# Performance work log

Measured on AMD Instinct MI355X. Metric: run time of the kernel, lower is better.

## Reference

```python
import jax, jax.numpy as jnp
import numpy as np
import math

KERNEL_SIZE = 11
SIGMA = 1.0
STABILIZATION = 1e-06


def _gauss_kernel(k, sigma):
    pad = k // 2
    coords = jnp.arange(k, dtype=jnp.float32) - pad
    yy, xx = jnp.meshgrid(coords, coords, indexing='ij')
    g = jnp.exp(-(xx ** 2 + yy ** 2) / (2.0 * sigma ** 2))
    return g / g.sum()


def _depthwise_gauss(x, g):
    # x: [B, C, H, W]; g: [K, K]. Zero 'SAME' padding matches nn.Unfold(padding=K//2).
    C = x.shape[1]
    k = g.shape[0]
    w = jnp.broadcast_to(g[None, None], (C, 1, k, k)).astype(x.dtype)
    return jax.lax.conv_general_dilated(
        x, w, window_strides=(1, 1), padding='SAME',
        feature_group_count=C,
        dimension_numbers=('NCHW', 'OIHW', 'NCHW'))


def setup_inputs() -> dict:
    key = jax.random.key(0)
    x = jax.random.normal(key, (16, 64, 256, 256), dtype=jnp.float32)
    return {"x": x}


def reference(x):
    g = _gauss_kernel(KERNEL_SIZE, SIGMA)
    # Weighted local mean and second moment; since sum(g)=1:
    # var = E_w[x^2] - (E_w[x])^2  ==  sum_w (x - mean)^2  (same math as the torch module)
    mean = _depthwise_gauss(x, g)
    ex2 = _depthwise_gauss(x * x, g)
    var = ex2 - mean * mean + STABILIZATION
    return jnp.sqrt(var)
```

## Files before the change

kernel.cpp:

```cpp
#include <hip/hip_runtime.h>
#include <math.h>


#define W        256
#define IMG_PIX  (W * W)
#define BANDH    64
#define LDSW     272

#define GW0 1.4867195e-06f
#define GW1 1.3383023e-04f
#define GW2 4.4318485e-03f
#define GW3 5.3990965e-02f
#define GW4 2.4197072e-01f
#define GW5 3.9894228e-01f

__device__ __forceinline__ float4 f4add(float4 a, float4 b) {
    return make_float4(a.x + b.x, a.y + b.y, a.z + b.z, a.w + b.w);
}
__device__ __forceinline__ float4 f4mul(float4 a, float4 b) {
    return make_float4(a.x * b.x, a.y * b.y, a.z * b.z, a.w * b.w);
}
__device__ __forceinline__ float4 f4scale(float g, float4 a) {
    return make_float4(g * a.x, g * a.y, g * a.z, g * a.w);
}
__device__ __forceinline__ float4 f4fma(float g, float4 a, float4 b) {
    return make_float4(fmaf(g, a.x, b.x), fmaf(g, a.y, b.y),
                       fmaf(g, a.z, b.z), fmaf(g, a.w, b.w));
}

__device__ __forceinline__ void lds_fence_hard() {
    __asm__ volatile("s_waitcnt lgkmcnt(0)" ::: "memory");
}
__device__ __forceinline__ void lds_fence_order() {
    __asm__ volatile("" ::: "memory");
}

__device__ __forceinline__ float4 load_row(const float* __restrict__ xi, int gr, int c) {
    if ((unsigned)gr < (unsigned)W)
        return *(const float4*)(xi + (size_t)gr * W + c);
    return make_float4(0.f, 0.f, 0.f, 0.f);
}

__device__ __forceinline__ void hconv4(float4 q0, float4 q1, float4 q2,
                                       float4 q3, float4 q4, float h[4]) {
    float f[20] = { q0.x, q0.y, q0.z, q0.w,  q1.x, q1.y, q1.z, q1.w,
                    q2.x, q2.y, q2.z, q2.w,  q3.x, q3.y, q3.z, q3.w,
                    q4.x, q4.y, q4.z, q4.w };
    #pragma unroll
    for (int j = 0; j < 4; ++j) {
        float s = GW5 * f[j + 8];
        s = fmaf(GW4, f[j + 7] + f[j + 9],  s);
        s = fmaf(GW3, f[j + 6] + f[j + 10], s);
        s = fmaf(GW2, f[j + 5] + f[j + 11], s);
        s = fmaf(GW1, f[j + 4] + f[j + 12], s);
        s = fmaf(GW0, f[j + 3] + f[j + 13], s);
        h[j] = s;
    }
}

template<int K>
__device__ __forceinline__ void row_step(const float* __restrict__ xi,
                                         float* __restrict__ oi,
                                         float4 (&xw)[11], float4& pf,
                                         float* __restrict__ b1,
                                         float* __restrict__ b2,
                                         int c, int grow) {
    constexpr int SN = (K + 10) % 11;
    xw[SN] = pf;
    float4 pn = load_row(xi, grow + 6, c);

    constexpr int SC = (K + 5) % 11;
    float4 xc = xw[SC];
    float4 v1 = f4scale(GW5, xc);
    float4 v2 = f4scale(GW5, f4mul(xc, xc));
    #define VPAIR(D, G) { constexpr int A_ = (K + 5 - (D)) % 11;                    \
                          constexpr int B_ = (K + 5 + (D)) % 11;                    \
                          float4 xa_ = xw[A_], xb_ = xw[B_];                        \
                          v1 = f4fma(G, f4add(xa_, xb_), v1);                       \
                          v2 = f4fma(G, f4add(f4mul(xa_, xa_), f4mul(xb_, xb_)), v2); }
    VPAIR(1, GW4) VPAIR(2, GW3) VPAIR(3, GW2) VPAIR(4, GW1) VPAIR(5, GW0)
    #undef VPAIR

    *(float4*)&b1[8 + c] = v1;
    *(float4*)&b2[8 + c] = v2;
    lds_fence_hard();

    float4 a0 = *(const float4*)&b1[c];
    float4 a1 = *(const float4*)&b1[c + 4];
    float4 a3 = *(const float4*)&b1[c + 12];
    float4 a4 = *(const float4*)&b1[c + 16];
    float4 d0 = *(const float4*)&b2[c];
    float4 d1 = *(const float4*)&b2[c + 4];
    float4 d3 = *(const float4*)&b2[c + 12];
    float4 d4 = *(const float4*)&b2[c + 16];
    lds_fence_order();

    float h1[4], h2[4];
    hconv4(a0, a1, v1, a3, a4, h1);
    hconv4(d0, d1, v2, d3, d4, h2);

    float4 o;
    o.x = sqrtf(fmaf(-h1[0], h1[0], h2[0]) + 1e-6f);
    o.y = sqrtf(fmaf(-h1[1], h1[1], h2[1]) + 1e-6f);
    o.z = sqrtf(fmaf(-h1[2], h1[2], h2[2]) + 1e-6f);
    o.w = sqrtf(fmaf(-h1[3], h1[3], h2[3]) + 1e-6f);
    *(float4*)(oi + (size_t)grow * W + c) = o;

    pf = pn;
}

__global__ __launch_bounds__(256, 4) void
local_std_kernel(const float* __restrict__ x, float* __restrict__ out) {
    __shared__ float buf[4][2][LDSW];

    const int t    = threadIdx.x;
    const int wv   = t >> 6;
    const int lane = t & 63;
    const int img  = blockIdx.x;
    const float* xi = x   + (size_t)img * IMG_PIX;
    float*       oi = out + (size_t)img * IMG_PIX;

    float* b1 = buf[wv][0];
    float* b2 = buf[wv][1];

    if (lane < 32) {
        int s = (lane >> 4) & 1;
        int q = lane & 15;
        int col = (q < 8) ? q : (256 + q);
        buf[wv][s][col] = 0.f;
    }

    const int c  = lane << 2;
    const int r0 = wv * BANDH;

    float4 xw[11];
    #pragma unroll
    for (int i = 0; i < 10; ++i)
        xw[i] = load_row(xi, r0 - 5 + i, c);
    xw[10] = make_float4(0.f, 0.f, 0.f, 0.f);
    float4 pf = load_row(xi, r0 + 5, c);

    #pragma unroll 1
    for (int ii = 0; ii < 6; ++ii) {
        const int base = ii * 11;
        #define STEP(k) if (base + (k) < BANDH) \
            row_step<(k)>(xi, oi, xw, pf, b1, b2, c, r0 + base + (k));
        STEP(0) STEP(1) STEP(2) STEP(3) STEP(4) STEP(5)
        STEP(6) STEP(7) STEP(8) STEP(9) STEP(10)
        #undef STEP
    }
}

extern "C" void kernel_launch(void* const* d_in, const int* in_sizes, int n_in,
                              void* d_out, int out_size, void* d_ws, size_t ws_size,
                              hipStream_t stream) {
    const float* x  = (const float*)d_in[0];
    float* out      = (float*)d_out;
    const int n_img = in_sizes[0] / IMG_PIX;
    local_std_kernel<<<dim3(n_img), 256, 0, stream>>>(x, out);
}
```

Before: 461.1 us.

## Replace LDS horizontal pass with wave shuffles and split each image across two blocks

The horizontal Gaussian pass now exchanges neighbouring column data through cross-lane shuffles instead of writing to and reading back from shared memory. Boundary lanes are masked with multipliers to keep zero padding. Each image is split into two blocks with 32-row bands per wave, doubling the grid, and launch bounds allow 8 blocks per CU. The goal is to drop the LDS round trip and raise occupancy, at the cost of extra halo rows recomputed per band and many shuffle instructions.

```diff
diff --git a/kernel.cpp b/kernel.cpp
--- a/kernel.cpp
+++ b/kernel.cpp
@@ -4,8 +4,7 @@
 
 #define W        256
 #define IMG_PIX  (W * W)
-#define BANDH    64
-#define LDSW     272
+#define BANDH    32
 
 #define GW0 1.4867195e-06f
 #define GW1 1.3383023e-04f
@@ -14,46 +13,55 @@
 #define GW4 2.4197072e-01f
 #define GW5 3.9894228e-01f
 
-__device__ __forceinline__ float4 f4add(float4 a, float4 b) {
-    return make_float4(a.x + b.x, a.y + b.y, a.z + b.z, a.w + b.w);
-}
-__device__ __forceinline__ float4 f4mul(float4 a, float4 b) {
-    return make_float4(a.x * b.x, a.y * b.y, a.z * b.z, a.w * b.w);
-}
-__device__ __forceinline__ float4 f4scale(float g, float4 a) {
-    return make_float4(g * a.x, g * a.y, g * a.z, g * a.w);
-}
-__device__ __forceinline__ float4 f4fma(float g, float4 a, float4 b) {
-    return make_float4(fmaf(g, a.x, b.x), fmaf(g, a.y, b.y),
-                       fmaf(g, a.z, b.z), fmaf(g, a.w, b.w));
+typedef float f4 __attribute__((ext_vector_type(4)));
+
+__device__ __forceinline__ f4 vfma(float g, f4 a, f4 c) {
+    f4 gv = {g, g, g, g};
+    return __builtin_elementwise_fma(gv, a, c);
 }
 
-__device__ __forceinline__ void lds_fence_hard() {
-    __asm__ volatile("s_waitcnt lgkmcnt(0)" ::: "memory");
-}
-__device__ __forceinline__ void lds_fence_order() {
-    __asm__ volatile("" ::: "memory");
+__device__ __forceinline__ f4 load_row(const float* __restrict__ xi, int gr, int c) {
+    if ((unsigned)gr < (unsigned)W)
+        return *(const f4*)(xi + (size_t)gr * W + c);
+    return (f4){0.f, 0.f, 0.f, 0.f};
 }
 
-__device__ __forceinline__ float4 load_row(const float* __restrict__ xi, int gr, int c) {
-    if ((unsigned)gr < (unsigned)W)
-        return *(const float4*)(xi + (size_t)gr * W + c);
-    return make_float4(0.f, 0.f, 0.f, 0.f);
+__device__ __forceinline__ f4 shfl_up1(f4 v) {
+    f4 r;
+    r.x = __shfl_up(v.x, 1);
+    r.y = __shfl_up(v.y, 1);
+    r.z = __shfl_up(v.z, 1);
+    r.w = __shfl_up(v.w, 1);
+    return r;
+}
+__device__ __forceinline__ f4 shfl_dn1(f4 v) {
+    f4 r;
+    r.x = __shfl_down(v.x, 1);
+    r.y = __shfl_down(v.y, 1);
+    r.z = __shfl_down(v.z, 1);
+    r.w = __shfl_down(v.w, 1);
+    return r;
 }
 
-__device__ __forceinline__ void hconv4(float4 q0, float4 q1, float4 q2,
-                                       float4 q3, float4 q4, float h[4]) {
-    float f[20] = { q0.x, q0.y, q0.z, q0.w,  q1.x, q1.y, q1.z, q1.w,
-                    q2.x, q2.y, q2.z, q2.w,  q3.x, q3.y, q3.z, q3.w,
-                    q4.x, q4.y, q4.z, q4.w };
+__device__ __forceinline__ void hpass(f4 v, float mu1, float mu2,
+                                      float md1, float md2, float h[4]) {
+    f4 L = shfl_up1(v);
+    float eL = __shfl_up(v.w, 2) * mu2;
+    f4 R = shfl_dn1(v);
+    float eR = __shfl_down(v.x, 2) * md2;
+    L *= mu1;
+    R *= md1;
+    float F[14] = { eL,  L.x, L.y, L.z, L.w,
+                    v.x, v.y, v.z, v.w,
+                    R.x, R.y, R.z, R.w,  eR };
     #pragma unroll
     for (int j = 0; j < 4; ++j) {
-        float s = GW5 * f[j + 8];
-        s = fmaf(GW4, f[j + 7] + f[j + 9],  s);
-        s = fmaf(GW3, f[j + 6] + f[j + 10], s);
-        s = fmaf(GW2, f[j + 5] + f[j + 11], s);
-        s = fmaf(GW1, f[j + 4] + f[j + 12], s);
-        s = fmaf(GW0, f[j + 3] + f[j + 13], s);
+        float s = GW5 * F[j + 5];
+        s = fmaf(GW4, F[j + 4] + F[j + 6],  s);
+        s = fmaf(GW3, F[j + 3] + F[j + 7],  s);
+        s = fmaf(GW2, F[j + 2] + F[j + 8],  s);
+        s = fmaf(GW1, F[j + 1] + F[j + 9],  s);
+        s = fmaf(GW0, F[j + 0] + F[j + 10], s);
         h[j] = s;
     }
 }
@@ -61,90 +69,72 @@
 template<int K>
 __device__ __forceinline__ void row_step(const float* __restrict__ xi,
                                          float* __restrict__ oi,
-                                         float4 (&xw)[11], float4& pf,
-                                         float* __restrict__ b1,
-                                         float* __restrict__ b2,
-                                         int c, int grow) {
+                                         f4 (&xw)[11], f4& pf,
+                                         int c, int grow,
+                                         float mu1, float mu2,
+                                         float md1, float md2) {
     constexpr int SN = (K + 10) % 11;
     xw[SN] = pf;
-    float4 pn = load_row(xi, grow + 6, c);
+    f4 pn = load_row(xi, grow + 6, c);
 
     constexpr int SC = (K + 5) % 11;
-    float4 xc = xw[SC];
-    float4 v1 = f4scale(GW5, xc);
-    float4 v2 = f4scale(GW5, f4mul(xc, xc));
-    #define VPAIR(D, G) { constexpr int A_ = (K + 5 - (D)) % 11;                    \
-                          constexpr int B_ = (K + 5 + (D)) % 11;                    \
-                          float4 xa_ = xw[A_], xb_ = xw[B_];                        \
-                          v1 = f4fma(G, f4add(xa_, xb_), v1);                       \
-                          v2 = f4fma(G, f4add(f4mul(xa_, xa_), f4mul(xb_, xb_)), v2); }
+    f4 xc = xw[SC];
+    f4 v1 = xc * GW5;
+    f4 v2 = (xc * xc) * GW5;
+    #define VPAIR(D, G) { constexpr int A_ = (K + 5 - (D)) % 11;                 \
+                          constexpr int B_ = (K + 5 + (D)) % 11;                 \
+                          f4 xa_ = xw[A_], xb_ = xw[B_];                         \
+                          v1 = vfma(G, xa_ + xb_, v1);                           \
+                          f4 sq_ = __builtin_elementwise_fma(xb_, xb_, xa_*xa_); \
+                          v2 = vfma(G, sq_, v2); }
     VPAIR(1, GW4) VPAIR(2, GW3) VPAIR(3, GW2) VPAIR(4, GW1) VPAIR(5, GW0)
     #undef VPAIR
 
-    *(float4*)&b1[8 + c] = v1;
-    *(float4*)&b2[8 + c] = v2;
-    lds_fence_hard();
+    float h1[4], h2[4];
+    hpass(v1, mu1, mu2, md1, md2, h1);
+    hpass(v2, mu1, mu2, md1, md2, h2);
 
-    float4 a0 = *(const float4*)&b1[c];
-    float4 a1 = *(const float4*)&b1[c + 4];
-    float4 a3 = *(const float4*)&b1[c + 12];
-    float4 a4 = *(const float4*)&b1[c + 16];
-    float4 d0 = *(const float4*)&b2[c];
-    float4 d1 = *(const float4*)&b2[c + 4];
-    float4 d3 = *(const float4*)&b2[c + 12];
-    float4 d4 = *(const float4*)&b2[c + 16];
-    lds_fence_order();
-
-    float h1[4], h2[4];
-    hconv4(a0, a1, v1, a3, a4, h1);
-    hconv4(d0, d1, v2, d3, d4, h2);
-
-    float4 o;
+    f4 o;
     o.x = sqrtf(fmaf(-h1[0], h1[0], h2[0]) + 1e-6f);
     o.y = sqrtf(fmaf(-h1[1], h1[1], h2[1]) + 1e-6f);
     o.z = sqrtf(fmaf(-h1[2], h1[2], h2[2]) + 1e-6f);
     o.w = sqrtf(fmaf(-h1[3], h1[3], h2[3]) + 1e-6f);
-    *(float4*)(oi + (size_t)grow * W + c) = o;
+    *(f4*)(oi + (size_t)grow * W + c) = o;
 
     pf = pn;
 }
 
-__global__ __launch_bounds__(256, 4) void
+__global__ __launch_bounds__(256, 8) void
 local_std_kernel(const float* __restrict__ x, float* __restrict__ out) {
-    __shared__ float buf[4][2][LDSW];
-
     const int t    = threadIdx.x;
     const int wv   = t >> 6;
     const int lane = t & 63;
-    const int img  = blockIdx.x;
+    const int bid  = blockIdx.x;
+    const int img  = bid >> 1;
+    const int half = bid & 1;
     const float* xi = x   + (size_t)img * IMG_PIX;
     float*       oi = out + (size_t)img * IMG_PIX;
 
-    float* b1 = buf[wv][0];
-    float* b2 = buf[wv][1];
+    const int c  = lane << 2;
+    const int r0 = half * (W / 2) + wv * BANDH;
 
-    if (lane < 32) {
-        int s = (lane >> 4) & 1;
-        int q = lane & 15;
-        int col = (q < 8) ? q : (256 + q);
-        buf[wv][s][col] = 0.f;
-    }
+    const float mu1 = (lane >= 1)  ? 1.f : 0.f;
+    const float mu2 = (lane >= 2)  ? 1.f : 0.f;
+    const float md1 = (lane <= 62) ? 1.f : 0.f;
+    const float md2 = (lane <= 61) ? 1.f : 0.f;
 
-    const int c  = lane << 2;
-    const int r0 = wv * BANDH;
-
-    float4 xw[11];
+    f4 xw[11];
     #pragma unroll
     for (int i = 0; i < 10; ++i)
         xw[i] = load_row(xi, r0 - 5 + i, c);
-    xw[10] = make_float4(0.f, 0.f, 0.f, 0.f);
-    float4 pf = load_row(xi, r0 + 5, c);
+    xw[10] = (f4){0.f, 0.f, 0.f, 0.f};
+    f4 pf = load_row(xi, r0 + 5, c);
 
     #pragma unroll 1
-    for (int ii = 0; ii < 6; ++ii) {
+    for (int ii = 0; ii < 3; ++ii) {
         const int base = ii * 11;
         #define STEP(k) if (base + (k) < BANDH) \
-            row_step<(k)>(xi, oi, xw, pf, b1, b2, c, r0 + base + (k));
+            row_step<(k)>(xi, oi, xw, pf, c, r0 + base + (k), mu1, mu2, md1, md2);
         STEP(0) STEP(1) STEP(2) STEP(3) STEP(4) STEP(5)
         STEP(6) STEP(7) STEP(8) STEP(9) STEP(10)
         #undef STEP
@@ -157,5 +147,5 @@
     const float* x  = (const float*)d_in[0];
     float* out      = (float*)d_out;
     const int n_img = in_sizes[0] / IMG_PIX;
-    local_std_kernel<<<dim3(n_img), 256, 0, stream>>>(x, out);
+    local_std_kernel<<<dim3(n_img * 2), 256, 0, stream>>>(x, out);
 }
```

New measurement: 978.6 us. +112.2%, slower.
